# Kernel optimization log

Hardware: AMD Instinct MI355X
Metric: run time of the kernel (lower is better)

Reference implementation:

```python
import jax, jax.numpy as jnp
import numpy as np

N = 100000
E = 1600000
IN_C = 128
HID = 64


def setup_inputs() -> dict:
    key = jax.random.key(0)
    ks = jax.random.split(key, 8)
    x = jax.random.normal(ks[0], (N, IN_C), dtype=jnp.float32)
    edge_index = jax.random.randint(ks[1], (2, E), 0, N, dtype=jnp.int64)
    # Glorot-ish init for faithfulness; exact init values don't matter for correctness baseline
    W1 = jax.random.normal(ks[2], (IN_C, HID), dtype=jnp.float32) / np.sqrt(IN_C)
    b1 = jnp.zeros((HID,), dtype=jnp.float32)
    W2 = jax.random.normal(ks[3], (HID, HID), dtype=jnp.float32) / np.sqrt(HID)
    b2 = jnp.zeros((HID,), dtype=jnp.float32)
    Wc = jax.random.normal(ks[4], (HID, 1), dtype=jnp.float32) / np.sqrt(HID)
    bc = jnp.zeros((1,), dtype=jnp.float32)
    return {"x": x, "edge_index": edge_index, "W1": W1, "b1": b1,
            "W2": W2, "b2": b2, "Wc": Wc, "bc": bc}


def _gcn_conv(x, W, b, src, dst, norm, n_nodes):
    # PyG GCNConv: h = x @ W; out[dst] += norm * h[src]; out += b
    h = x @ W                                  # [N, out_c]
    msg = h[src] * norm[:, None]               # [E+N, out_c] gather + scale
    out = jax.ops.segment_sum(msg, dst, num_segments=n_nodes)  # scatter-add
    return out + b


def reference(x, edge_index, W1, b1, W2, b2, Wc, bc):
    n = x.shape[0]
    loop = jnp.arange(n, dtype=edge_index.dtype)
    src = jnp.concatenate([edge_index[0], loop])   # add self-loops (PyG default)
    dst = jnp.concatenate([edge_index[1], loop])
    # symmetric normalization: deg over destination (col) including self-loops
    deg = jax.ops.segment_sum(jnp.ones_like(dst, dtype=x.dtype), dst, num_segments=n)
    dinv = jnp.where(deg > 0, jax.lax.rsqrt(deg), 0.0)
    norm = dinv[src] * dinv[dst]                   # [E+N]

    h = jax.nn.relu(_gcn_conv(x, W1, b1, src, dst, norm, n))
    h = jax.nn.relu(_gcn_conv(h, W2, b2, src, dst, norm, n))
    logits = (h @ Wc + bc)[:, 0]                   # squeeze(-1)
    return logits
```

## Files before the change

kernel.cpp:

```cpp
#include <hip/hip_runtime.h>
#include <hip/hip_fp16.h>


#define IN_C 128
#define HID  64
#define CAP  64
#define NBUCKET 256
#define BCHUNK  391
#define BUCKET_CAP 8192
#define EPB 2048

typedef __attribute__((ext_vector_type(4))) _Float16 half4;
typedef __attribute__((ext_vector_type(8))) _Float16 half8;
typedef __attribute__((ext_vector_type(4))) float f32x4;

__global__ void k_zero_i32(int* __restrict__ p, int n) {
    int i = blockIdx.x * blockDim.x + threadIdx.x;
    if (i < n) p[i] = 0;
}

__global__ void k_partition(const int* __restrict__ ei, int* __restrict__ cursor,
                            int2* __restrict__ ebuf, int E) {
    __shared__ int2 stage[EPB];
    __shared__ unsigned char sbkt[EPB];
    __shared__ int cnt[NBUCKET];
    __shared__ int pfx[NBUCKET];
    __shared__ int bstart[NBUCKET];
    __shared__ int gbase[NBUCKET];

    int t = threadIdx.x;
    int e0 = blockIdx.x * EPB;
    cnt[t] = 0;
    __syncthreads();

    int  myb[EPB / 256];
    int2 myv[EPB / 256];
    #pragma unroll
    for (int i = 0; i < EPB / 256; ++i) {
        int e = e0 + i * 256 + t;
        int b = -1; int2 v = make_int2(0, 0);
        if (e < E) {
            v.x = ei[e];
            v.y = ei[E + e];
            b = v.y / BCHUNK;
            atomicAdd(&cnt[b], 1);
        }
        myb[i] = b; myv[i] = v;
    }
    __syncthreads();

    int c = cnt[t];
    pfx[t] = c;
    __syncthreads();
    #pragma unroll
    for (int off = 1; off < NBUCKET; off <<= 1) {
        int u = (t >= off) ? pfx[t - off] : 0;
        __syncthreads();
        pfx[t] += u;
        __syncthreads();
    }
    bstart[t] = pfx[t] - c;
    gbase[t]  = atomicAdd(&cursor[t], c);
    cnt[t] = 0;
    __syncthreads();

    #pragma unroll
    for (int i = 0; i < EPB / 256; ++i) {
        int b = myb[i];
        if (b >= 0) {
            int pos = bstart[b] + atomicAdd(&cnt[b], 1);
            stage[pos] = myv[i];
            sbkt[pos]  = (unsigned char)b;
        }
    }
    __syncthreads();

    int total = pfx[NBUCKET - 1];
    for (int i = t; i < total; i += 256) {
        int b = sbkt[i];
        int off = gbase[b] + (i - bstart[b]);
        if (off < BUCKET_CAP)
            ebuf[(long)b * BUCKET_CAP + off] = stage[i];
    }
}

__global__ void k_fill_bucket(const int2* __restrict__ ebuf, const int* __restrict__ cursor,
                              int* __restrict__ deg, float* __restrict__ dinv,
                              int* __restrict__ pairs, int n) {
    __shared__ int lcur[BCHUNK];
    int t = threadIdx.x;
    int b = blockIdx.x;
    int lo = b * BCHUNK;
    int hi = min(n, lo + BCHUNK);
    for (int i = t; i < BCHUNK; i += 256) lcur[i] = 0;
    __syncthreads();

    int cnt = min(cursor[b], BUCKET_CAP);
    const int2* p = ebuf + (long)b * BUCKET_CAP;
    for (int i = t; i < cnt; i += 256) {
        int2 v = p[i];
        int pos = atomicAdd(&lcur[v.y - lo], 1);
        if (pos < CAP) pairs[(long)v.y * CAP + pos] = v.x;
    }
    __syncthreads();
    for (int i = lo + t; i < hi; i += 256) {
        int d = lcur[i - lo];
        deg[i]  = d;
        dinv[i] = rsqrtf((float)(d + 1));
    }
}

__launch_bounds__(256)
__global__ void k_gemm1_mfma(const float* __restrict__ X, const float* __restrict__ W,
                             const float* __restrict__ dinv, _Float16* __restrict__ H,
                             int n) {
    int lane = threadIdx.x & 63;
    int m    = lane & 15;
    int quad = lane >> 4;
    int wid  = blockIdx.x * (blockDim.x >> 6) + (threadIdx.x >> 6);
    int nwav = gridDim.x * (blockDim.x >> 6);

    half8 wf[4][4];
    #pragma unroll
    for (int ks = 0; ks < 4; ++ks)
        #pragma unroll
        for (int ct = 0; ct < 4; ++ct)
            #pragma unroll
            for (int j = 0; j < 8; ++j)
                wf[ct][ks][j] = (_Float16)W[(ks * 32 + quad * 8 + j) * 64 + ct * 16 + m];

    int ntile = (n + 15) >> 4;
    for (int tile = wid; tile < ntile; tile += nwav) {
        int row0 = tile << 4;
        const float* xr = X + (long)min(row0 + m, n - 1) * IN_C;

        float4 xa[4], xb[4];
        #pragma unroll
        for (int ks = 0; ks < 4; ++ks) {
            xa[ks] = *(const float4*)&xr[ks * 32 + quad * 8];
            xb[ks] = *(const float4*)&xr[ks * 32 + quad * 8 + 4];
        }
        half8 af[4];
        #pragma unroll
        for (int ks = 0; ks < 4; ++ks) {
            af[ks][0] = (_Float16)xa[ks].x; af[ks][1] = (_Float16)xa[ks].y;
            af[ks][2] = (_Float16)xa[ks].z; af[ks][3] = (_Float16)xa[ks].w;
            af[ks][4] = (_Float16)xb[ks].x; af[ks][5] = (_Float16)xb[ks].y;
            af[ks][6] = (_Float16)xb[ks].z; af[ks][7] = (_Float16)xb[ks].w;
        }

        f32x4 acc0 = {0.f, 0.f, 0.f, 0.f}, acc1 = acc0, acc2 = acc0, acc3 = acc0;
        #pragma unroll
        for (int ks = 0; ks < 4; ++ks) {
            acc0 = __builtin_amdgcn_mfma_f32_16x16x32_f16(af[ks], wf[0][ks], acc0, 0, 0, 0);
            acc1 = __builtin_amdgcn_mfma_f32_16x16x32_f16(af[ks], wf[1][ks], acc1, 0, 0, 0);
            acc2 = __builtin_amdgcn_mfma_f32_16x16x32_f16(af[ks], wf[2][ks], acc2, 0, 0, 0);
            acc3 = __builtin_amdgcn_mfma_f32_16x16x32_f16(af[ks], wf[3][ks], acc3, 0, 0, 0);
        }

        #pragma unroll
        for (int r = 0; r < 4; ++r) {
            int row = row0 + quad * 4 + r;
            if (row < n) {
                float dv = dinv[row];
                _Float16* hp = H + (long)row * 64 + m;
                hp[0]  = (_Float16)(dv * acc0[r]);
                hp[16] = (_Float16)(dv * acc1[r]);
                hp[32] = (_Float16)(dv * acc2[r]);
                hp[48] = (_Float16)(dv * acc3[r]);
            }
        }
    }
}

__device__ __forceinline__ void gather_sum8(const _Float16* __restrict__ H,
                                            int4 q, int cnt, int gb, int h, int c8,
                                            float acc[8]) {
    int jj = 0;
    for (; jj + 16 <= cnt; jj += 16) {
        int bl = gb + (jj >> 2) + (h << 1);
        int s0 = __shfl(q.x, bl, 64);
        int s1 = __shfl(q.y, bl, 64);
        int s2 = __shfl(q.z, bl, 64);
        int s3 = __shfl(q.w, bl, 64);
        int s4 = __shfl(q.x, bl + 1, 64);
        int s5 = __shfl(q.y, bl + 1, 64);
        int s6 = __shfl(q.z, bl + 1, 64);
        int s7 = __shfl(q.w, bl + 1, 64);
        half8 v0 = *(const half8*)&H[(long)s0 * 64 + c8];
        half8 v1 = *(const half8*)&H[(long)s1 * 64 + c8];
        half8 v2 = *(const half8*)&H[(long)s2 * 64 + c8];
        half8 v3 = *(const half8*)&H[(long)s3 * 64 + c8];
        half8 v4 = *(const half8*)&H[(long)s4 * 64 + c8];
        half8 v5 = *(const half8*)&H[(long)s5 * 64 + c8];
        half8 v6 = *(const half8*)&H[(long)s6 * 64 + c8];
        half8 v7 = *(const half8*)&H[(long)s7 * 64 + c8];
        #pragma unroll
        for (int k = 0; k < 8; ++k) {
            acc[k] += (float)v0[k] + (float)v1[k] + (float)v2[k] + (float)v3[k]
                    + (float)v4[k] + (float)v5[k] + (float)v6[k] + (float)v7[k];
        }
    }
    if (jj < cnt) {
        int bl = gb + (jj >> 2) + (h << 1);
        int s[8];
        s[0] = __shfl(q.x, bl, 64);
        s[1] = __shfl(q.y, bl, 64);
        s[2] = __shfl(q.z, bl, 64);
        s[3] = __shfl(q.w, bl, 64);
        s[4] = __shfl(q.x, bl + 1, 64);
        s[5] = __shfl(q.y, bl + 1, 64);
        s[6] = __shfl(q.z, bl + 1, 64);
        s[7] = __shfl(q.w, bl + 1, 64);
        #pragma unroll
        for (int u = 0; u < 8; ++u) {
            int slot = jj + 8 * h + u;
            bool ok = slot < cnt;
            int sc = ok ? s[u] : 0;
            half8 v = *(const half8*)&H[(long)sc * 64 + c8];
            float w = ok ? 1.f : 0.f;
            #pragma unroll
            for (int k = 0; k < 8; ++k)
                acc[k] = fmaf((float)v[k], w, acc[k]);
        }
    }
}

__launch_bounds__(256)
__global__ void k_gather_mfma(const _Float16* __restrict__ H, const int* __restrict__ pairs,
                              const int* __restrict__ deg, const float* __restrict__ dinv,
                              const float* __restrict__ b1, const float* __restrict__ W2,
                              _Float16* __restrict__ OUT, int n) {
    __shared__ _Float16 Rs[16 * 72];

    int t    = threadIdx.x;
    int lane = t & 63;
    int m    = lane & 15;
    int quad = lane >> 4;
    int wave = t >> 6;
    int l16  = t & 15;
    int nb   = t >> 4;
    int node0 = blockIdx.x * 16;
    int node  = node0 + nb;
    int nodeC  = (node < n) ? node : (n - 1);
    int gb = lane & ~15;
    int h  = l16 >> 3;
    int c8 = (l16 & 7) * 8;

    half8 wf[2];
    #pragma unroll
    for (int ks = 0; ks < 2; ++ks)
        #pragma unroll
        for (int j = 0; j < 8; ++j)
            wf[ks][j] = (_Float16)W2[(ks * 32 + quad * 8 + j) * 64 + wave * 16 + m];

    float di = dinv[nodeC];
    int cnt  = min(deg[nodeC], CAP);
    int4 q = make_int4(0, 0, 0, 0);
    if (l16 * 4 < cnt) q = *(const int4*)&pairs[(long)nodeC * CAP + l16 * 4];

    half8 h0 = *(const half8*)&H[(long)nodeC * 64 + c8];
    float ws = (h == 0) ? 1.f : 0.f;
    float acc[8];
    #pragma unroll
    for (int k = 0; k < 8; ++k) acc[k] = ws * (float)h0[k];

    gather_sum8(H, q, cnt, gb, h, c8, acc);

    #pragma unroll
    for (int k = 0; k < 8; ++k) acc[k] += __shfl_xor(acc[k], 8, 64);

    float4 bba = *(const float4*)&b1[c8];
    float4 bbb = *(const float4*)&b1[c8 + 4];
    half8 r8;
    r8[0] = (_Float16)fmaxf(fmaf(di, acc[0], bba.x), 0.f);
    r8[1] = (_Float16)fmaxf(fmaf(di, acc[1], bba.y), 0.f);
    r8[2] = (_Float16)fmaxf(fmaf(di, acc[2], bba.z), 0.f);
    r8[3] = (_Float16)fmaxf(fmaf(di, acc[3], bba.w), 0.f);
    r8[4] = (_Float16)fmaxf(fmaf(di, acc[4], bbb.x), 0.f);
    r8[5] = (_Float16)fmaxf(fmaf(di, acc[5], bbb.y), 0.f);
    r8[6] = (_Float16)fmaxf(fmaf(di, acc[6], bbb.z), 0.f);
    r8[7] = (_Float16)fmaxf(fmaf(di, acc[7], bbb.w), 0.f);
    if (h == 0) *(half8*)&Rs[nb * 72 + c8] = r8;
    __syncthreads();

    half8 af[2];
    #pragma unroll
    for (int ks = 0; ks < 2; ++ks)
        af[ks] = *(const half8*)&Rs[m * 72 + ks * 32 + quad * 8];

    f32x4 o = {0.f, 0.f, 0.f, 0.f};
    o = __builtin_amdgcn_mfma_f32_16x16x32_f16(af[0], wf[0], o, 0, 0, 0);
    o = __builtin_amdgcn_mfma_f32_16x16x32_f16(af[1], wf[1], o, 0, 0, 0);

    #pragma unroll
    for (int rr = 0; rr < 4; ++rr) {
        int row = node0 + quad * 4 + rr;
        if (row < n) {
            float dv = dinv[row];
            OUT[(long)row * 64 + wave * 16 + m] = (_Float16)(dv * o[rr]);
        }
    }
}

__launch_bounds__(256)
__global__ void k_gather_head(const _Float16* __restrict__ H, const int* __restrict__ pairs,
                              const int* __restrict__ deg, const float* __restrict__ dinv,
                              const float* __restrict__ b2, const float* __restrict__ Wc,
                              const float* __restrict__ bc, float* __restrict__ OUT, int n) {
    int t = blockIdx.x * blockDim.x + threadIdx.x;
    int node = t >> 4;
    int l16  = threadIdx.x & 15;
    int gb   = (threadIdx.x & 63) & ~15;
    if (node >= n) return;
    int h  = l16 >> 3;
    int c8 = (l16 & 7) * 8;

    float di = dinv[node];
    int cnt  = min(deg[node], CAP);
    int4 q = make_int4(0, 0, 0, 0);
    if (l16 * 4 < cnt) q = *(const int4*)&pairs[(long)node * CAP + l16 * 4];

    half8 h0 = *(const half8*)&H[(long)node * 64 + c8];
    float ws = (h == 0) ? 1.f : 0.f;
    float acc[8];
    #pragma unroll
    for (int k = 0; k < 8; ++k) acc[k] = ws * (float)h0[k];

    gather_sum8(H, q, cnt, gb, h, c8, acc);

    #pragma unroll
    for (int k = 0; k < 8; ++k) acc[k] += __shfl_xor(acc[k], 8, 64);

    float4 bba = *(const float4*)&b2[c8];
    float4 bbb = *(const float4*)&b2[c8 + 4];
    float4 wca = *(const float4*)&Wc[c8];
    float4 wcb = *(const float4*)&Wc[c8 + 4];
    float v = fmaxf(fmaf(di, acc[0], bba.x), 0.f) * wca.x
            + fmaxf(fmaf(di, acc[1], bba.y), 0.f) * wca.y
            + fmaxf(fmaf(di, acc[2], bba.z), 0.f) * wca.z
            + fmaxf(fmaf(di, acc[3], bba.w), 0.f) * wca.w
            + fmaxf(fmaf(di, acc[4], bbb.x), 0.f) * wcb.x
            + fmaxf(fmaf(di, acc[5], bbb.y), 0.f) * wcb.y
            + fmaxf(fmaf(di, acc[6], bbb.z), 0.f) * wcb.z
            + fmaxf(fmaf(di, acc[7], bbb.w), 0.f) * wcb.w;
    v += __shfl_down(v, 8, 16);
    v += __shfl_down(v, 4, 16);
    v += __shfl_down(v, 2, 16);
    v += __shfl_down(v, 1, 16);
    if (l16 == 0) OUT[node] = 0.5f * v + bc[0];
}

extern "C" void kernel_launch(void* const* d_in, const int* in_sizes, int n_in,
                              void* d_out, int out_size, void* d_ws, size_t ws_size,
                              hipStream_t stream) {
    const float* x  = (const float*)d_in[0];
    const int*   ei = (const int*)d_in[1];
    const float* W1 = (const float*)d_in[2];
    const float* b1 = (const float*)d_in[3];
    const float* W2 = (const float*)d_in[4];
    const float* b2 = (const float*)d_in[5];
    const float* Wc = (const float*)d_in[6];
    const float* bc = (const float*)d_in[7];
    float* out = (float*)d_out;

    const int n = in_sizes[0] / IN_C;
    const int E = in_sizes[1] / 2;

    char* w = (char*)d_ws;
    auto alloc = [&](size_t bytes) { char* r = w; w += (bytes + 255) & ~(size_t)255; return r; };
    int*      deg    = (int*)alloc((size_t)n * 4);
    float*    dinv   = (float*)alloc((size_t)n * 4);
    int*      pairs  = (int*)alloc((size_t)n * CAP * 4);
    _Float16* A16    = (_Float16*)alloc((size_t)n * HID * 2);
    _Float16* B16    = (_Float16*)alloc((size_t)n * HID * 2);
    int*      cursor = (int*)alloc(NBUCKET * 4);
    int2*     ebuf   = (int2*)alloc((size_t)NBUCKET * BUCKET_CAP * 8);

    const int BS = 256;
    dim3 blk(BS);
    auto grid_items = [&](long items) { return dim3((unsigned)((items + BS - 1) / BS)); };

    k_zero_i32<<<dim3(1), blk, 0, stream>>>(cursor, NBUCKET);
    k_partition<<<dim3((unsigned)((E + EPB - 1) / EPB)), blk, 0, stream>>>(ei, cursor, ebuf, E);
    k_fill_bucket<<<dim3(NBUCKET), blk, 0, stream>>>(ebuf, cursor, deg, dinv, pairs, n);

    k_gemm1_mfma<<<dim3(1024), blk, 0, stream>>>(x, W1, dinv, A16, n);

    k_gather_mfma<<<grid_items((long)n * 16), blk, 0, stream>>>(
        A16, pairs, deg, dinv, b1, W2, B16, n);

    k_gather_head<<<grid_items((long)n * 16), blk, 0, stream>>>(
        B16, pairs, deg, dinv, b2, Wc, bc, out, n);
}
```

Measured before the change: 213.8 us.

## Replace bucketed partition CSR build with direct global-atomic adjacency fill

Drops the two-pass bucket partition (partition into 256 destination buckets, then a per-bucket shared-memory fill) and replaces it with a single kernel that does a global atomicAdd on deg[dst] per edge and writes src into a fixed-capacity slot list. The dinv array goes away; each consumer recomputes rsqrt(deg+1) inline. This removes a kernel launch, the intermediate edge buffer traffic and the shared-memory staging. In exchange it relies on contended global atomics with scattered writes, and adds a memset of deg.

Result: slower. 298.2 us (+39.5%).

```diff
diff --git a/kernel.cpp b/kernel.cpp
--- a/kernel.cpp
+++ b/kernel.cpp
@@ -5,114 +5,25 @@
 #define IN_C 128
 #define HID  64
 #define CAP  64
-#define NBUCKET 256
-#define BCHUNK  391
-#define BUCKET_CAP 8192
-#define EPB 2048
 
 typedef __attribute__((ext_vector_type(4))) _Float16 half4;
 typedef __attribute__((ext_vector_type(8))) _Float16 half8;
 typedef __attribute__((ext_vector_type(4))) float f32x4;
 
-__global__ void k_zero_i32(int* __restrict__ p, int n) {
-    int i = blockIdx.x * blockDim.x + threadIdx.x;
-    if (i < n) p[i] = 0;
-}
-
-__global__ void k_partition(const int* __restrict__ ei, int* __restrict__ cursor,
-                            int2* __restrict__ ebuf, int E) {
-    __shared__ int2 stage[EPB];
-    __shared__ unsigned char sbkt[EPB];
-    __shared__ int cnt[NBUCKET];
-    __shared__ int pfx[NBUCKET];
-    __shared__ int bstart[NBUCKET];
-    __shared__ int gbase[NBUCKET];
-
-    int t = threadIdx.x;
-    int e0 = blockIdx.x * EPB;
-    cnt[t] = 0;
-    __syncthreads();
-
-    int  myb[EPB / 256];
-    int2 myv[EPB / 256];
-    #pragma unroll
-    for (int i = 0; i < EPB / 256; ++i) {
-        int e = e0 + i * 256 + t;
-        int b = -1; int2 v = make_int2(0, 0);
-        if (e < E) {
-            v.x = ei[e];
-            v.y = ei[E + e];
-            b = v.y / BCHUNK;
-            atomicAdd(&cnt[b], 1);
-        }
-        myb[i] = b; myv[i] = v;
-    }
-    __syncthreads();
-
-    int c = cnt[t];
-    pfx[t] = c;
-    __syncthreads();
-    #pragma unroll
-    for (int off = 1; off < NBUCKET; off <<= 1) {
-        int u = (t >= off) ? pfx[t - off] : 0;
-        __syncthreads();
-        pfx[t] += u;
-        __syncthreads();
-    }
-    bstart[t] = pfx[t] - c;
-    gbase[t]  = atomicAdd(&cursor[t], c);
-    cnt[t] = 0;
-    __syncthreads();
-
-    #pragma unroll
-    for (int i = 0; i < EPB / 256; ++i) {
-        int b = myb[i];
-        if (b >= 0) {
-            int pos = bstart[b] + atomicAdd(&cnt[b], 1);
-            stage[pos] = myv[i];
-            sbkt[pos]  = (unsigned char)b;
-        }
-    }
-    __syncthreads();
-
-    int total = pfx[NBUCKET - 1];
-    for (int i = t; i < total; i += 256) {
-        int b = sbkt[i];
-        int off = gbase[b] + (i - bstart[b]);
-        if (off < BUCKET_CAP)
-            ebuf[(long)b * BUCKET_CAP + off] = stage[i];
-    }
-}
-
-__global__ void k_fill_bucket(const int2* __restrict__ ebuf, const int* __restrict__ cursor,
-                              int* __restrict__ deg, float* __restrict__ dinv,
-                              int* __restrict__ pairs, int n) {
-    __shared__ int lcur[BCHUNK];
-    int t = threadIdx.x;
-    int b = blockIdx.x;
-    int lo = b * BCHUNK;
-    int hi = min(n, lo + BCHUNK);
-    for (int i = t; i < BCHUNK; i += 256) lcur[i] = 0;
-    __syncthreads();
-
-    int cnt = min(cursor[b], BUCKET_CAP);
-    const int2* p = ebuf + (long)b * BUCKET_CAP;
-    for (int i = t; i < cnt; i += 256) {
-        int2 v = p[i];
-        int pos = atomicAdd(&lcur[v.y - lo], 1);
-        if (pos < CAP) pairs[(long)v.y * CAP + pos] = v.x;
-    }
-    __syncthreads();
-    for (int i = lo + t; i < hi; i += 256) {
-        int d = lcur[i - lo];
-        deg[i]  = d;
-        dinv[i] = rsqrtf((float)(d + 1));
+__global__ void k_build_csr(const int* __restrict__ ei, int* __restrict__ deg,
+                            int* __restrict__ pairs, int E) {
+    int e = blockIdx.x * blockDim.x + threadIdx.x;
+    if (e < E) {
+        int src = ei[e];
+        int dst = ei[E + e];
+        int pos = atomicAdd(&deg[dst], 1);
+        if (pos < CAP) pairs[(long)dst * CAP + pos] = src;
     }
 }
 
 __launch_bounds__(256)
 __global__ void k_gemm1_mfma(const float* __restrict__ X, const float* __restrict__ W,
-                             const float* __restrict__ dinv, _Float16* __restrict__ H,
+                             const int* __restrict__ deg, _Float16* __restrict__ H,
                              int n) {
     int lane = threadIdx.x & 63;
     int m    = lane & 15;
@@ -162,7 +73,7 @@
         for (int r = 0; r < 4; ++r) {
             int row = row0 + quad * 4 + r;
             if (row < n) {
-                float dv = dinv[row];
+                float dv = rsqrtf((float)(deg[row] + 1));
                 _Float16* hp = H + (long)row * 64 + m;
                 hp[0]  = (_Float16)(dv * acc0[r]);
                 hp[16] = (_Float16)(dv * acc1[r]);
@@ -228,7 +139,7 @@
 
 __launch_bounds__(256)
 __global__ void k_gather_mfma(const _Float16* __restrict__ H, const int* __restrict__ pairs,
-                              const int* __restrict__ deg, const float* __restrict__ dinv,
+                              const int* __restrict__ deg,
                               const float* __restrict__ b1, const float* __restrict__ W2,
                               _Float16* __restrict__ OUT, int n) {
     __shared__ _Float16 Rs[16 * 72];
@@ -254,8 +165,9 @@
         for (int j = 0; j < 8; ++j)
             wf[ks][j] = (_Float16)W2[(ks * 32 + quad * 8 + j) * 64 + wave * 16 + m];
 
-    float di = dinv[nodeC];
-    int cnt  = min(deg[nodeC], CAP);
+    int d    = deg[nodeC];
+    float di = rsqrtf((float)(d + 1));
+    int cnt  = min(d, CAP);
     int4 q = make_int4(0, 0, 0, 0);
     if (l16 * 4 < cnt) q = *(const int4*)&pairs[(long)nodeC * CAP + l16 * 4];
 
@@ -297,7 +209,7 @@
     for (int rr = 0; rr < 4; ++rr) {
         int row = node0 + quad * 4 + rr;
         if (row < n) {
-            float dv = dinv[row];
+            float dv = rsqrtf((float)(deg[row] + 1));
             OUT[(long)row * 64 + wave * 16 + m] = (_Float16)(dv * o[rr]);
         }
     }
@@ -305,7 +217,7 @@
 
 __launch_bounds__(256)
 __global__ void k_gather_head(const _Float16* __restrict__ H, const int* __restrict__ pairs,
-                              const int* __restrict__ deg, const float* __restrict__ dinv,
+                              const int* __restrict__ deg,
                               const float* __restrict__ b2, const float* __restrict__ Wc,
                               const float* __restrict__ bc, float* __restrict__ OUT, int n) {
     int t = blockIdx.x * blockDim.x + threadIdx.x;
@@ -316,8 +228,9 @@
     int h  = l16 >> 3;
     int c8 = (l16 & 7) * 8;
 
-    float di = dinv[node];
-    int cnt  = min(deg[node], CAP);
+    int d    = deg[node];
+    float di = rsqrtf((float)(d + 1));
+    int cnt  = min(d, CAP);
     int4 q = make_int4(0, 0, 0, 0);
     if (l16 * 4 < cnt) q = *(const int4*)&pairs[(long)node * CAP + l16 * 4];
 
@@ -370,26 +283,22 @@
     char* w = (char*)d_ws;
     auto alloc = [&](size_t bytes) { char* r = w; w += (bytes + 255) & ~(size_t)255; return r; };
     int*      deg    = (int*)alloc((size_t)n * 4);
-    float*    dinv   = (float*)alloc((size_t)n * 4);
     int*      pairs  = (int*)alloc((size_t)n * CAP * 4);
     _Float16* A16    = (_Float16*)alloc((size_t)n * HID * 2);
     _Float16* B16    = (_Float16*)alloc((size_t)n * HID * 2);
-    int*      cursor = (int*)alloc(NBUCKET * 4);
-    int2*     ebuf   = (int2*)alloc((size_t)NBUCKET * BUCKET_CAP * 8);
 
     const int BS = 256;
     dim3 blk(BS);
     auto grid_items = [&](long items) { return dim3((unsigned)((items + BS - 1) / BS)); };
 
-    k_zero_i32<<<dim3(1), blk, 0, stream>>>(cursor, NBUCKET);
-    k_partition<<<dim3((unsigned)((E + EPB - 1) / EPB)), blk, 0, stream>>>(ei, cursor, ebuf, E);
-    k_fill_bucket<<<dim3(NBUCKET), blk, 0, stream>>>(ebuf, cursor, deg, dinv, pairs, n);
-
-    k_gemm1_mfma<<<dim3(1024), blk, 0, stream>>>(x, W1, dinv, A16, n);
+    hipMemsetAsync(deg, 0, (size_t)n * 4, stream);
+    k_build_csr<<<grid_items(E), blk, 0, stream>>>(ei, deg, pairs, E);
+
+    k_gemm1_mfma<<<dim3(1024), blk, 0, stream>>>(x, W1, deg, A16, n);
 
     k_gather_mfma<<<grid_items((long)n * 16), blk, 0, stream>>>(
-        A16, pairs, deg, dinv, b1, W2, B16, n);
+        A16, pairs, deg, b1, W2, B16, n);
 
     k_gather_head<<<grid_items((long)n * 16), blk, 0, stream>>>(
-        B16, pairs, deg, dinv, b2, Wc, bc, out, n);
-}
+        B16, pairs, deg, b2, Wc, bc, out, n);
+}
```
